# Optimization experiments

Hardware: AMD Instinct MI355X
Metric: run time of the kernel (lower is better)

## Reference

```python
import jax, jax.numpy as jnp
import numpy as np

MEDNUM = 50000
FEATDIM = 128
NNZ = 3200000
N = 2 * MEDNUM  # adjacency is over cat([mEmbed, mEmbed])


def setup_inputs() -> dict:
    key = jax.random.key(0)
    k1, k2, k3, k4, k5 = jax.random.split(key, 5)
    vals = jax.random.uniform(k1, (NNZ,), dtype=jnp.float32)
    mEmbed = jax.random.normal(k2, (MEDNUM, FEATDIM), dtype=jnp.float32)
    inter = jax.random.normal(k3, (1,), dtype=jnp.float32)
    row_idx = jax.random.randint(k4, (NNZ,), 0, N, dtype=jnp.int32)
    col_idx = jax.random.randint(k5, (NNZ,), 0, N, dtype=jnp.int32)
    return {"vals": vals, "mEmbed": mEmbed, "inter": inter,
            "row_idx": row_idx, "col_idx": col_idx}


def _gcn_layer(vals, row_idx, col_idx, embeds):
    # spmm(adj, embeds) via gather + weighted segment-sum, then LeakyReLU(0.5)
    gathered = embeds[col_idx] * vals[:, None]          # [E, F]
    agg = jax.ops.segment_sum(gathered, row_idx, num_segments=N)  # [N, F]
    return jnp.where(agg >= 0, agg, 0.5 * agg)          # LeakyReLU(negative_slope=0.5)


def reference(vals, mEmbed, inter, row_idx, col_idx):
    embeds1 = jnp.concatenate([mEmbed, mEmbed], axis=0)  # [2*mednum, F]
    # Source quirk: lats1 is never extended, so both iterations use embeds1.
    tem1 = jax.nn.relu(_gcn_layer(vals, row_idx, col_idx, embeds1))
    gnnEmbeds1 = tem1 + tem1                              # sum of two identical layers
    m1 = gnnEmbeds1[:MEDNUM]
    m2 = gnnEmbeds1[MEDNUM:]
    return inter * m1 + (1.0 - inter) * m2
```

## Files before the change

kernel.cpp:

```cpp
#include <hip/hip_runtime.h>

#define MEDNUM 50000
#define FEATDIM 128
#define NNZ 3200000
#define NBUCK 1563
#define SLAB 2304
#define PART_BLOCKS 250
#define PART_E 12800
#define PART_T 1024
#define PART_K 12
#define PART_TAIL 512
#define CAP SLAB

#define OFF_CUR    0
#define OFF_SCALE  1600
#define OFF_QT     51600
#define OFF_RECS   3251600


__global__ __launch_bounds__(256) void toint8_kernel(const float* __restrict__ mEmbed,
                                                     unsigned short* __restrict__ qt,
                                                     float* __restrict__ scales,
                                                     int* __restrict__ gcur) {
    int g = blockIdx.x * 256 + threadIdx.x;
    if (g < NBUCK) gcur[g] = g * SLAB;

    int row = blockIdx.x * 4 + (threadIdx.x >> 6);
    int lane = threadIdx.x & 63;
    if (row >= MEDNUM) return;
    float2 f = ((const float2*)(mEmbed + (long long)row * FEATDIM))[lane];
    float m = fmaxf(fabsf(f.x), fabsf(f.y));
    for (int o = 32; o > 0; o >>= 1) m = fmaxf(m, __shfl_xor(m, o, 64));
    float inv = (m > 0.f) ? 127.f / m : 0.f;
    float s   = (m > 0.f) ? m / 127.f : 0.f;
    int q0 = __float2int_rn(f.x * inv) + 128;
    int q1 = __float2int_rn(f.y * inv) + 128;
    qt[(long long)row * 64 + ((lane & 15) * 4 + (lane >> 4))] =
        (unsigned short)((q0 & 0xff) | ((q1 & 0xff) << 8));
    if (lane == 0) scales[row] = s;
}

__global__ __launch_bounds__(PART_T, 4) void part_kernel(const float* __restrict__ vals,
                                                         const int* __restrict__ row_idx,
                                                         const int* __restrict__ col_idx,
                                                         const float* __restrict__ scales,
                                                         int* __restrict__ gcur,
                                                         unsigned long long* __restrict__ recs) {
    __shared__ unsigned long long lrec[PART_E];
    __shared__ int lcnt[NBUCK];
    __shared__ int gstart[NBUCK];
    __shared__ int wsum[16];

    int tid = threadIdx.x;
    int base = blockIdx.x * PART_E;

    for (int i = tid; i < NBUCK; i += PART_T) lcnt[i] = 0;
    __syncthreads();

    unsigned long long rec[PART_K];
    unsigned long long rtail = 0;
    int have_tail = (tid < PART_TAIL);
    {
        int rr[PART_K], cc[PART_K];
        float vv[PART_K];
#pragma unroll
        for (int k = 0; k < PART_K; k++) {
            int e = base + k * PART_T + tid;
            rr[k] = __builtin_nontemporal_load(row_idx + e);
            cc[k] = __builtin_nontemporal_load(col_idx + e);
            vv[k] = __builtin_nontemporal_load(vals + e);
        }
        int rt = 0, ct = 0; float vt = 0.f;
        if (have_tail) {
            int e = base + PART_K * PART_T + tid;
            rt = __builtin_nontemporal_load(row_idx + e);
            ct = __builtin_nontemporal_load(col_idx + e);
            vt = __builtin_nontemporal_load(vals + e);
        }
        float ss[PART_K];
#pragma unroll
        for (int k = 0; k < PART_K; k++) {
            cc[k] = (cc[k] >= MEDNUM) ? cc[k] - MEDNUM : cc[k];
            ss[k] = scales[cc[k]];
        }
        float st = 0.f;
        if (have_tail) {
            ct = (ct >= MEDNUM) ? ct - MEDNUM : ct;
            st = scales[ct];
        }
#pragma unroll
        for (int k = 0; k < PART_K; k++) {
            int r = rr[k], half = 0;
            if (r >= MEDNUM) { r -= MEDNUM; half = 1; }
            float vp = vv[k] * ss[k];
            int b = r >> 5;
            int rib = (r & 31) | (half << 5);
            rec[k] = ((unsigned long long)__float_as_uint(vp) << 32)
                   | ((unsigned long long)(b >> 10) << 63)
                   | ((unsigned int)(b & 0x3FF) << 22)
                   | ((unsigned int)rib << 16)
                   | (unsigned int)cc[k];
            atomicAdd(&lcnt[b], 1);
        }
        if (have_tail) {
            int r = rt, half = 0;
            if (r >= MEDNUM) { r -= MEDNUM; half = 1; }
            float vp = vt * st;
            int b = r >> 5;
            int rib = (r & 31) | (half << 5);
            rtail = ((unsigned long long)__float_as_uint(vp) << 32)
                  | ((unsigned long long)(b >> 10) << 63)
                  | ((unsigned int)(b & 0x3FF) << 22)
                  | ((unsigned int)rib << 16)
                  | (unsigned int)ct;
            atomicAdd(&lcnt[b], 1);
        }
    }
    __syncthreads();

    int i0 = tid * 2;
    int c0 = 0, c1 = 0;
    if (i0 < NBUCK)     c0 = lcnt[i0];
    if (i0 + 1 < NBUCK) c1 = lcnt[i0 + 1];
    int s = c0 + c1;
    int x = s;
#pragma unroll
    for (int d = 1; d < 64; d <<= 1) {
        int t = __shfl_up(x, d, 64);
        if ((tid & 63) >= d) x += t;
    }
    int wave = tid >> 6, lane = tid & 63;
    if (lane == 63) wsum[wave] = x;
    __syncthreads();
    if (tid == 0) {
        int acc = 0;
#pragma unroll
        for (int w = 0; w < 16; w++) { int t = wsum[w]; wsum[w] = acc; acc += t; }
    }
    __syncthreads();
    int excl = wsum[wave] + x - s;

    {
        int e = excl;
        if (i0 < NBUCK) {
            if (c0 > 0) gstart[i0] = atomicAdd(&gcur[i0], c0) - e;
            lcnt[i0] = e;
            e += c0;
        }
        if (i0 + 1 < NBUCK) {
            if (c1 > 0) gstart[i0 + 1] = atomicAdd(&gcur[i0 + 1], c1) - e;
            lcnt[i0 + 1] = e;
            e += c1;
        }
    }
    __syncthreads();

#pragma unroll
    for (int k = 0; k < PART_K; k++) {
        unsigned long long r = rec[k];
        int b = (int)(((r >> 53) & 0x400u) | ((r >> 22) & 0x3FFu));
        int pos = atomicAdd(&lcnt[b], 1);
        lrec[pos] = r;
    }
    if (have_tail) {
        unsigned long long r = rtail;
        int b = (int)(((r >> 53) & 0x400u) | ((r >> 22) & 0x3FFu));
        int pos = atomicAdd(&lcnt[b], 1);
        lrec[pos] = r;
    }
    __syncthreads();

#pragma unroll
    for (int k = 0; k < PART_K; k++) {
        int j = k * PART_T + tid;
        unsigned long long r = lrec[j];
        int b = (int)(((r >> 53) & 0x400u) | ((r >> 22) & 0x3FFu));
        recs[gstart[b] + j] = r & 0x7FFFFFFFFFFFFFFFULL;
    }
    if (have_tail) {
        int j = PART_K * PART_T + tid;
        unsigned long long r = lrec[j];
        int b = (int)(((r >> 53) & 0x400u) | ((r >> 22) & 0x3FFu));
        recs[gstart[b] + j] = r & 0x7FFFFFFFFFFFFFFFULL;
    }
}

__device__ __forceinline__ void accum8_body(const unsigned int p[8],
                                            const unsigned short* __restrict__ qt,
                                            unsigned int flo,
                                            float acc[8], float& sv) {
    unsigned long long w[8];
#pragma unroll
    for (int q = 0; q < 8; q++)
        w[q] = *(const unsigned long long*)((const char*)qt
                   + (((p[q] & 0xffffu) << 7) | flo));
#pragma unroll
    for (int q = 0; q < 8; q++) {
        float v = __uint_as_float(p[q] & 0xffff0000u);
        sv += v;
        unsigned int wlo = (unsigned int)w[q], whi = (unsigned int)(w[q] >> 32);
        acc[0] = fmaf(v, (float)(wlo & 0xffu),         acc[0]);
        acc[1] = fmaf(v, (float)((wlo >> 8) & 0xffu),  acc[1]);
        acc[2] = fmaf(v, (float)((wlo >> 16) & 0xffu), acc[2]);
        acc[3] = fmaf(v, (float)(wlo >> 24),           acc[3]);
        acc[4] = fmaf(v, (float)(whi & 0xffu),         acc[4]);
        acc[5] = fmaf(v, (float)((whi >> 8) & 0xffu),  acc[5]);
        acc[6] = fmaf(v, (float)((whi >> 16) & 0xffu), acc[6]);
        acc[7] = fmaf(v, (float)(whi >> 24),           acc[7]);
    }
}

__device__ __forceinline__ void seg_to_pair(int s, int e,
                                            const unsigned int* __restrict__ st4,
                                            const unsigned short* __restrict__ qt,
                                            int qw, unsigned int flo,
                                            float& rx, float& ry) {
    float acc[8], sv;
#pragma unroll
    for (int x = 0; x < 8; x++) acc[x] = 0.f;
    sv = 0.f;
    int i = s;
    for (; i + 32 <= e; i += 32) {
        unsigned int p[8];
#pragma unroll
        for (int q = 0; q < 8; q++) p[q] = st4[i + q * 4 + qw];
        accum8_body(p, qt, flo, acc, sv);
    }
    if (i < e) {
        unsigned int p[8];
#pragma unroll
        for (int q = 0; q < 8; q++) {
            int j = i + q * 4 + qw;
            p[q] = (j < e) ? st4[j] : 0u;
        }
        accum8_body(p, qt, flo, acc, sv);
    }
#pragma unroll
    for (int x = 0; x < 8; x++) {
        acc[x] += __shfl_xor(acc[x], 16, 64);
        acc[x] += __shfl_xor(acc[x], 32, 64);
    }
    sv += __shfl_xor(sv, 16, 64);
    sv += __shfl_xor(sv, 32, 64);
    float sx = (qw & 2) ? ((qw & 1) ? acc[6] : acc[4]) : ((qw & 1) ? acc[2] : acc[0]);
    float sy = (qw & 2) ? ((qw & 1) ? acc[7] : acc[5]) : ((qw & 1) ? acc[3] : acc[1]);
    rx = fmaxf(fmaf(-128.f, sv, sx), 0.f);
    ry = fmaxf(fmaf(-128.f, sv, sy), 0.f);
}

__global__ __launch_bounds__(512, 6) void agg_kernel(const int* __restrict__ gcur,
                                                     const unsigned long long* __restrict__ recs,
                                                     const unsigned short* __restrict__ qt,
                                                     const float* __restrict__ inter,
                                                     float* __restrict__ out) {
    __shared__ unsigned long long slab8[CAP];
    __shared__ unsigned int st4[CAP];
    __shared__ int cnt[64];
    __shared__ int bas[65];
    int b = blockIdx.x, tid = threadIdx.x;
    long long gs = (long long)b * SLAB;
    int n = gcur[b] - b * SLAB;
    if (n > CAP) n = CAP;

    if (tid < 64) cnt[tid] = 0;
    __syncthreads();
    for (int j = tid; j < n; j += 512) {
        unsigned long long r = __builtin_nontemporal_load(recs + gs + j);
        slab8[j] = r;
        atomicAdd(&cnt[(int)((r >> 16) & 63)], 1);
    }
    __syncthreads();
    if (tid < 64) {
        int v = cnt[tid];
        int x = v;
#pragma unroll
        for (int d = 1; d < 64; d <<= 1) {
            int tmp = __shfl_up(x, d, 64);
            if (tid >= d) x += tmp;
        }
        bas[tid] = x - v;
        if (tid == 63) bas[64] = x;
        cnt[tid] = x - v;
    }
    __syncthreads();
    for (int j = tid; j < n; j += 512) {
        unsigned long long r = slab8[j];
        int rib = (int)((r >> 16) & 63);
        int p = atomicAdd(&cnt[rib], 1);
        unsigned int vb = (unsigned int)(r >> 32);
        vb = (vb + 0x7fffu + ((vb >> 16) & 1u)) & 0xffff0000u;
        st4[p] = ((unsigned int)(r & 0xffff)) | vb;
    }
    __syncthreads();
    float t = inter[0];
    float s1 = 2.f * t, s2 = 2.f * (1.f - t);
    int wave = tid >> 6, lane = tid & 63;
    int qw = lane >> 4;
    unsigned int flo = (unsigned int)((lane & 15) << 3);
#pragma unroll 1
    for (int i2 = 0; i2 < 4; i2++) {
        int rib0 = wave * 4 + i2;
        int frow = b * 32 + rib0;
        if (frow >= MEDNUM) break;
        float ax, ay, cx, cy;
        seg_to_pair(bas[rib0],      bas[rib0 + 1],  st4, qt, qw, flo, ax, ay);
        seg_to_pair(bas[rib0 + 32], bas[rib0 + 33], st4, qt, qw, flo, cx, cy);
        float ox = s1 * ax + s2 * cx;
        float oy = s1 * ay + s2 * cy;
        unsigned long long packed =
            (unsigned long long)__float_as_uint(ox)
          | ((unsigned long long)__float_as_uint(oy) << 32);
        __builtin_nontemporal_store(packed,
            (unsigned long long*)(out + (long long)frow * FEATDIM + lane * 2));
    }
}

extern "C" void kernel_launch(void* const* d_in, const int* in_sizes, int n_in,
                              void* d_out, int out_size, void* d_ws, size_t ws_size,
                              hipStream_t stream) {
    const float* vals    = (const float*)d_in[0];
    const float* mEmbed  = (const float*)d_in[1];
    const float* inter   = (const float*)d_in[2];
    const int*   row_idx = (const int*)d_in[3];
    const int*   col_idx = (const int*)d_in[4];
    float* out = (float*)d_out;

    int* ws = (int*)d_ws;
    int* gcur = ws + OFF_CUR;
    float* scales = (float*)(ws + OFF_SCALE);
    unsigned short* qt = (unsigned short*)(ws + OFF_QT);
    unsigned long long* recs = (unsigned long long*)(ws + OFF_RECS);

    toint8_kernel<<<(MEDNUM + 3) / 4, 256, 0, stream>>>(mEmbed, qt, scales, gcur);
    part_kernel<<<PART_BLOCKS, PART_T, 0, stream>>>(vals, row_idx, col_idx, scales, gcur, recs);
    agg_kernel<<<NBUCK, 512, 0, stream>>>(gcur, recs, qt, inter, out);
}
```

Before: 198.2 us.

## Replace int8 per-row-scaled embedding table with fp16 and fma_mix accumulation

Stores the embedding table as fp16 instead of int8 with per-row scales, and accumulates with v_fma_mix_f32 straight from packed halves. This removes the scale gather in the partition kernel, the byte-extract and convert work, and the offset-correction sum in the aggregation. In exchange each gathered row is twice as many bytes (16-byte loads per lane), and the inner unroll drops from 8 to 6 edges per step. Accuracy should also improve over the int8 quantisation.

```diff
diff --git a/kernel.cpp b/kernel.cpp
--- a/kernel.cpp
+++ b/kernel.cpp
@@ -1,4 +1,5 @@
 #include <hip/hip_runtime.h>
+#include <hip/hip_fp16.h>
 
 #define MEDNUM 50000
 #define FEATDIM 128
@@ -18,9 +19,17 @@
 #define OFF_RECS   3251600
 
 
-__global__ __launch_bounds__(256) void toint8_kernel(const float* __restrict__ mEmbed,
-                                                     unsigned short* __restrict__ qt,
-                                                     float* __restrict__ scales,
+__device__ __forceinline__ void fmamix_lo(float& acc, float v, unsigned int w) {
+    asm("v_fma_mix_f32 %0, %1, %2, %0 op_sel:[0,0,0] op_sel_hi:[0,1,0]"
+        : "+v"(acc) : "v"(v), "v"(w));
+}
+__device__ __forceinline__ void fmamix_hi(float& acc, float v, unsigned int w) {
+    asm("v_fma_mix_f32 %0, %1, %2, %0 op_sel:[0,1,0] op_sel_hi:[0,1,0]"
+        : "+v"(acc) : "v"(v), "v"(w));
+}
+
+__global__ __launch_bounds__(256) void tofp16_kernel(const float* __restrict__ mEmbed,
+                                                     unsigned int* __restrict__ qt,
                                                      int* __restrict__ gcur) {
     int g = blockIdx.x * 256 + threadIdx.x;
     if (g < NBUCK) gcur[g] = g * SLAB;
@@ -29,21 +38,14 @@
     int lane = threadIdx.x & 63;
     if (row >= MEDNUM) return;
     float2 f = ((const float2*)(mEmbed + (long long)row * FEATDIM))[lane];
-    float m = fmaxf(fabsf(f.x), fabsf(f.y));
-    for (int o = 32; o > 0; o >>= 1) m = fmaxf(m, __shfl_xor(m, o, 64));
-    float inv = (m > 0.f) ? 127.f / m : 0.f;
-    float s   = (m > 0.f) ? m / 127.f : 0.f;
-    int q0 = __float2int_rn(f.x * inv) + 128;
-    int q1 = __float2int_rn(f.y * inv) + 128;
-    qt[(long long)row * 64 + ((lane & 15) * 4 + (lane >> 4))] =
-        (unsigned short)((q0 & 0xff) | ((q1 & 0xff) << 8));
-    if (lane == 0) scales[row] = s;
+    unsigned int h0 = __half_as_ushort(__float2half(f.x));
+    unsigned int h1 = __half_as_ushort(__float2half(f.y));
+    qt[(long long)row * 64 + 4 * (lane & 15) + (lane >> 4)] = h0 | (h1 << 16);
 }
 
 __global__ __launch_bounds__(PART_T, 4) void part_kernel(const float* __restrict__ vals,
                                                          const int* __restrict__ row_idx,
                                                          const int* __restrict__ col_idx,
-                                                         const float* __restrict__ scales,
                                                          int* __restrict__ gcur,
                                                          unsigned long long* __restrict__ recs) {
     __shared__ unsigned long long lrec[PART_E];
@@ -77,25 +79,14 @@
             ct = __builtin_nontemporal_load(col_idx + e);
             vt = __builtin_nontemporal_load(vals + e);
         }
-        float ss[PART_K];
 #pragma unroll
         for (int k = 0; k < PART_K; k++) {
             cc[k] = (cc[k] >= MEDNUM) ? cc[k] - MEDNUM : cc[k];
-            ss[k] = scales[cc[k]];
-        }
-        float st = 0.f;
-        if (have_tail) {
-            ct = (ct >= MEDNUM) ? ct - MEDNUM : ct;
-            st = scales[ct];
-        }
-#pragma unroll
-        for (int k = 0; k < PART_K; k++) {
             int r = rr[k], half = 0;
             if (r >= MEDNUM) { r -= MEDNUM; half = 1; }
-            float vp = vv[k] * ss[k];
             int b = r >> 5;
             int rib = (r & 31) | (half << 5);
-            rec[k] = ((unsigned long long)__float_as_uint(vp) << 32)
+            rec[k] = ((unsigned long long)__float_as_uint(vv[k]) << 32)
                    | ((unsigned long long)(b >> 10) << 63)
                    | ((unsigned int)(b & 0x3FF) << 22)
                    | ((unsigned int)rib << 16)
@@ -103,12 +94,12 @@
             atomicAdd(&lcnt[b], 1);
         }
         if (have_tail) {
+            ct = (ct >= MEDNUM) ? ct - MEDNUM : ct;
             int r = rt, half = 0;
             if (r >= MEDNUM) { r -= MEDNUM; half = 1; }
-            float vp = vt * st;
             int b = r >> 5;
             int rib = (r & 31) | (half << 5);
-            rtail = ((unsigned long long)__float_as_uint(vp) << 32)
+            rtail = ((unsigned long long)__float_as_uint(vt) << 32)
                   | ((unsigned long long)(b >> 10) << 63)
                   | ((unsigned int)(b & 0x3FF) << 22)
                   | ((unsigned int)rib << 16)
@@ -185,72 +176,62 @@
     }
 }
 
-__device__ __forceinline__ void accum8_body(const unsigned int p[8],
-                                            const unsigned short* __restrict__ qt,
+__device__ __forceinline__ void accum6_body(const unsigned int p[6],
+                                            const unsigned int* __restrict__ qt,
                                             unsigned int flo,
-                                            float acc[8], float& sv) {
-    unsigned long long w[8];
-#pragma unroll
-    for (int q = 0; q < 8; q++)
-        w[q] = *(const unsigned long long*)((const char*)qt
-                   + (((p[q] & 0xffffu) << 7) | flo));
-#pragma unroll
-    for (int q = 0; q < 8; q++) {
+                                            float acc[8]) {
+    uint4 W[6];
+#pragma unroll
+    for (int q = 0; q < 6; q++)
+        W[q] = *(const uint4*)((const char*)qt + (((p[q] & 0xffffu) << 8) | flo));
+#pragma unroll
+    for (int q = 0; q < 6; q++) {
         float v = __uint_as_float(p[q] & 0xffff0000u);
-        sv += v;
-        unsigned int wlo = (unsigned int)w[q], whi = (unsigned int)(w[q] >> 32);
-        acc[0] = fmaf(v, (float)(wlo & 0xffu),         acc[0]);
-        acc[1] = fmaf(v, (float)((wlo >> 8) & 0xffu),  acc[1]);
-        acc[2] = fmaf(v, (float)((wlo >> 16) & 0xffu), acc[2]);
-        acc[3] = fmaf(v, (float)(wlo >> 24),           acc[3]);
-        acc[4] = fmaf(v, (float)(whi & 0xffu),         acc[4]);
-        acc[5] = fmaf(v, (float)((whi >> 8) & 0xffu),  acc[5]);
-        acc[6] = fmaf(v, (float)((whi >> 16) & 0xffu), acc[6]);
-        acc[7] = fmaf(v, (float)(whi >> 24),           acc[7]);
+        fmamix_lo(acc[0], v, W[q].x); fmamix_hi(acc[1], v, W[q].x);
+        fmamix_lo(acc[2], v, W[q].y); fmamix_hi(acc[3], v, W[q].y);
+        fmamix_lo(acc[4], v, W[q].z); fmamix_hi(acc[5], v, W[q].z);
+        fmamix_lo(acc[6], v, W[q].w); fmamix_hi(acc[7], v, W[q].w);
     }
 }
 
 __device__ __forceinline__ void seg_to_pair(int s, int e,
                                             const unsigned int* __restrict__ st4,
-                                            const unsigned short* __restrict__ qt,
+                                            const unsigned int* __restrict__ qt,
                                             int qw, unsigned int flo,
                                             float& rx, float& ry) {
-    float acc[8], sv;
+    float acc[8];
 #pragma unroll
     for (int x = 0; x < 8; x++) acc[x] = 0.f;
-    sv = 0.f;
     int i = s;
-    for (; i + 32 <= e; i += 32) {
-        unsigned int p[8];
-#pragma unroll
-        for (int q = 0; q < 8; q++) p[q] = st4[i + q * 4 + qw];
-        accum8_body(p, qt, flo, acc, sv);
+    for (; i + 24 <= e; i += 24) {
+        unsigned int p[6];
+#pragma unroll
+        for (int q = 0; q < 6; q++) p[q] = st4[i + q * 4 + qw];
+        accum6_body(p, qt, flo, acc);
     }
     if (i < e) {
-        unsigned int p[8];
-#pragma unroll
-        for (int q = 0; q < 8; q++) {
+        unsigned int p[6];
+#pragma unroll
+        for (int q = 0; q < 6; q++) {
             int j = i + q * 4 + qw;
             p[q] = (j < e) ? st4[j] : 0u;
         }
-        accum8_body(p, qt, flo, acc, sv);
+        accum6_body(p, qt, flo, acc);
     }
 #pragma unroll
     for (int x = 0; x < 8; x++) {
         acc[x] += __shfl_xor(acc[x], 16, 64);
         acc[x] += __shfl_xor(acc[x], 32, 64);
     }
-    sv += __shfl_xor(sv, 16, 64);
-    sv += __shfl_xor(sv, 32, 64);
     float sx = (qw & 2) ? ((qw & 1) ? acc[6] : acc[4]) : ((qw & 1) ? acc[2] : acc[0]);
     float sy = (qw & 2) ? ((qw & 1) ? acc[7] : acc[5]) : ((qw & 1) ? acc[3] : acc[1]);
-    rx = fmaxf(fmaf(-128.f, sv, sx), 0.f);
-    ry = fmaxf(fmaf(-128.f, sv, sy), 0.f);
+    rx = fmaxf(sx, 0.f);
+    ry = fmaxf(sy, 0.f);
 }
 
 __global__ __launch_bounds__(512, 6) void agg_kernel(const int* __restrict__ gcur,
                                                      const unsigned long long* __restrict__ recs,
-                                                     const unsigned short* __restrict__ qt,
+                                                     const unsigned int* __restrict__ qt,
                                                      const float* __restrict__ inter,
                                                      float* __restrict__ out) {
     __shared__ unsigned long long slab8[CAP];
@@ -296,7 +277,7 @@
     float s1 = 2.f * t, s2 = 2.f * (1.f - t);
     int wave = tid >> 6, lane = tid & 63;
     int qw = lane >> 4;
-    unsigned int flo = (unsigned int)((lane & 15) << 3);
+    unsigned int flo = (unsigned int)((lane & 15) << 4);
 #pragma unroll 1
     for (int i2 = 0; i2 < 4; i2++) {
         int rib0 = wave * 4 + i2;
@@ -327,11 +308,10 @@
 
     int* ws = (int*)d_ws;
     int* gcur = ws + OFF_CUR;
-    float* scales = (float*)(ws + OFF_SCALE);
-    unsigned short* qt = (unsigned short*)(ws + OFF_QT);
+    unsigned int* qt = (unsigned int*)(ws + OFF_QT);
     unsigned long long* recs = (unsigned long long*)(ws + OFF_RECS);
 
-    toint8_kernel<<<(MEDNUM + 3) / 4, 256, 0, stream>>>(mEmbed, qt, scales, gcur);
-    part_kernel<<<PART_BLOCKS, PART_T, 0, stream>>>(vals, row_idx, col_idx, scales, gcur, recs);
+    tofp16_kernel<<<(MEDNUM + 3) / 4, 256, 0, stream>>>(mEmbed, qt, gcur);
+    part_kernel<<<PART_BLOCKS, PART_T, 0, stream>>>(vals, row_idx, col_idx, gcur, recs);
     agg_kernel<<<NBUCK, 512, 0, stream>>>(gcur, recs, qt, inter, out);
 }
```

Result: slower. 244.4 us (+23.3%).

## Split quantized embedding table into two column halves processed in separate passes

Applied to the files above, without the earlier changes.

The int8 embedding table is split into two halves by column index (rows below and above 25000), and the record column field now carries a half bit. The aggregation kernel bins edges by destination row and column half, then runs two passes over the halves, summing partial results before the ReLU and output scaling. Each pass gathers from a half-size table, which is meant to improve cache locality for the random gathers. In exchange it adds twice as many segment loops, a smaller inner unroll (4 instead of 8 gathers in flight), and extra scan and binning work.

```diff
diff --git a/kernel.cpp b/kernel.cpp
--- a/kernel.cpp
+++ b/kernel.cpp
@@ -1,6 +1,7 @@
 #include <hip/hip_runtime.h>
 
 #define MEDNUM 50000
+#define COLH 25000
 #define FEATDIM 128
 #define NNZ 3200000
 #define NBUCK 1563
@@ -35,7 +36,9 @@
     float s   = (m > 0.f) ? m / 127.f : 0.f;
     int q0 = __float2int_rn(f.x * inv) + 128;
     int q1 = __float2int_rn(f.y * inv) + 128;
-    qt[(long long)row * 64 + ((lane & 15) * 4 + (lane >> 4))] =
+    int h = (row >= COLH);
+    int rm = row - (h ? COLH : 0);
+    qt[h * 1600000 + rm * 64 + ((lane & 15) * 4 + (lane >> 4))] =
         (unsigned short)((q0 & 0xff) | ((q1 & 0xff) << 8));
     if (lane == 0) scales[row] = s;
 }
@@ -95,11 +98,14 @@
             float vp = vv[k] * ss[k];
             int b = r >> 5;
             int rib = (r & 31) | (half << 5);
+            int c = cc[k];
+            int ch = (c >= COLH);
+            unsigned int colfield = (unsigned int)(c - (ch ? COLH : 0)) | ((unsigned int)ch << 15);
             rec[k] = ((unsigned long long)__float_as_uint(vp) << 32)
                    | ((unsigned long long)(b >> 10) << 63)
                    | ((unsigned int)(b & 0x3FF) << 22)
                    | ((unsigned int)rib << 16)
-                   | (unsigned int)cc[k];
+                   | colfield;
             atomicAdd(&lcnt[b], 1);
         }
         if (have_tail) {
@@ -108,11 +114,13 @@
             float vp = vt * st;
             int b = r >> 5;
             int rib = (r & 31) | (half << 5);
+            int ch = (ct >= COLH);
+            unsigned int colfield = (unsigned int)(ct - (ch ? COLH : 0)) | ((unsigned int)ch << 15);
             rtail = ((unsigned long long)__float_as_uint(vp) << 32)
                   | ((unsigned long long)(b >> 10) << 63)
                   | ((unsigned int)(b & 0x3FF) << 22)
                   | ((unsigned int)rib << 16)
-                  | (unsigned int)ct;
+                  | colfield;
             atomicAdd(&lcnt[b], 1);
         }
     }
@@ -185,17 +193,16 @@
     }
 }
 
-__device__ __forceinline__ void accum8_body(const unsigned int p[8],
-                                            const unsigned short* __restrict__ qt,
+__device__ __forceinline__ void accum4_body(const unsigned int p[4],
+                                            const unsigned char* __restrict__ qb,
                                             unsigned int flo,
                                             float acc[8], float& sv) {
-    unsigned long long w[8];
-#pragma unroll
-    for (int q = 0; q < 8; q++)
-        w[q] = *(const unsigned long long*)((const char*)qt
-                   + (((p[q] & 0xffffu) << 7) | flo));
-#pragma unroll
-    for (int q = 0; q < 8; q++) {
+    unsigned long long w[4];
+#pragma unroll
+    for (int q = 0; q < 4; q++)
+        w[q] = *(const unsigned long long*)(qb + (((p[q] & 0x7fffu) << 7) | flo));
+#pragma unroll
+    for (int q = 0; q < 4; q++) {
         float v = __uint_as_float(p[q] & 0xffff0000u);
         sv += v;
         unsigned int wlo = (unsigned int)w[q], whi = (unsigned int)(w[q] >> 32);
@@ -210,30 +217,29 @@
     }
 }
 
-__device__ __forceinline__ void seg_to_pair(int s, int e,
-                                            const unsigned int* __restrict__ st4,
-                                            const unsigned short* __restrict__ qt,
-                                            int qw, unsigned int flo,
-                                            float& rx, float& ry) {
-    float acc[8], sv;
+__device__ __forceinline__ void seg_pair(int s, int e,
+                                         const unsigned int* __restrict__ st4,
+                                         const unsigned char* __restrict__ qb,
+                                         int qw, unsigned int flo,
+                                         float& rx, float& ry) {
+    float acc[8], sv = 0.f;
 #pragma unroll
     for (int x = 0; x < 8; x++) acc[x] = 0.f;
-    sv = 0.f;
     int i = s;
-    for (; i + 32 <= e; i += 32) {
-        unsigned int p[8];
-#pragma unroll
-        for (int q = 0; q < 8; q++) p[q] = st4[i + q * 4 + qw];
-        accum8_body(p, qt, flo, acc, sv);
+    for (; i + 16 <= e; i += 16) {
+        unsigned int p[4];
+#pragma unroll
+        for (int q = 0; q < 4; q++) p[q] = st4[i + q * 4 + qw];
+        accum4_body(p, qb, flo, acc, sv);
     }
     if (i < e) {
-        unsigned int p[8];
-#pragma unroll
-        for (int q = 0; q < 8; q++) {
+        unsigned int p[4];
+#pragma unroll
+        for (int q = 0; q < 4; q++) {
             int j = i + q * 4 + qw;
             p[q] = (j < e) ? st4[j] : 0u;
         }
-        accum8_body(p, qt, flo, acc, sv);
+        accum4_body(p, qb, flo, acc, sv);
     }
 #pragma unroll
     for (int x = 0; x < 8; x++) {
@@ -244,8 +250,8 @@
     sv += __shfl_xor(sv, 32, 64);
     float sx = (qw & 2) ? ((qw & 1) ? acc[6] : acc[4]) : ((qw & 1) ? acc[2] : acc[0]);
     float sy = (qw & 2) ? ((qw & 1) ? acc[7] : acc[5]) : ((qw & 1) ? acc[3] : acc[1]);
-    rx = fmaxf(fmaf(-128.f, sv, sx), 0.f);
-    ry = fmaxf(fmaf(-128.f, sv, sy), 0.f);
+    rx = fmaf(-128.f, sv, sx);
+    ry = fmaf(-128.f, sv, sy);
 }
 
 __global__ __launch_bounds__(512, 6) void agg_kernel(const int* __restrict__ gcur,
@@ -255,38 +261,43 @@
                                                      float* __restrict__ out) {
     __shared__ unsigned long long slab8[CAP];
     __shared__ unsigned int st4[CAP];
-    __shared__ int cnt[64];
-    __shared__ int bas[65];
+    __shared__ int cnt[128];
+    __shared__ int bas[129];
     int b = blockIdx.x, tid = threadIdx.x;
     long long gs = (long long)b * SLAB;
     int n = gcur[b] - b * SLAB;
     if (n > CAP) n = CAP;
 
-    if (tid < 64) cnt[tid] = 0;
+    if (tid < 128) cnt[tid] = 0;
     __syncthreads();
     for (int j = tid; j < n; j += 512) {
         unsigned long long r = __builtin_nontemporal_load(recs + gs + j);
         slab8[j] = r;
-        atomicAdd(&cnt[(int)((r >> 16) & 63)], 1);
+        int bin = (int)((r >> 16) & 63) | (((int)(r >> 15) & 1) << 6);
+        atomicAdd(&cnt[bin], 1);
     }
     __syncthreads();
     if (tid < 64) {
-        int v = cnt[tid];
-        int x = v;
+        int c0 = cnt[2 * tid], c1 = cnt[2 * tid + 1];
+        int s = c0 + c1;
+        int x = s;
 #pragma unroll
         for (int d = 1; d < 64; d <<= 1) {
             int tmp = __shfl_up(x, d, 64);
             if (tid >= d) x += tmp;
         }
-        bas[tid] = x - v;
-        if (tid == 63) bas[64] = x;
-        cnt[tid] = x - v;
+        int excl = x - s;
+        bas[2 * tid] = excl;
+        bas[2 * tid + 1] = excl + c0;
+        if (tid == 63) bas[128] = x;
+        cnt[2 * tid] = excl;
+        cnt[2 * tid + 1] = excl + c0;
     }
     __syncthreads();
     for (int j = tid; j < n; j += 512) {
         unsigned long long r = slab8[j];
-        int rib = (int)((r >> 16) & 63);
-        int p = atomicAdd(&cnt[rib], 1);
+        int bin = (int)((r >> 16) & 63) | (((int)(r >> 15) & 1) << 6);
+        int p = atomicAdd(&cnt[bin], 1);
         unsigned int vb = (unsigned int)(r >> 32);
         vb = (vb + 0x7fffu + ((vb >> 16) & 1u)) & 0xffff0000u;
         st4[p] = ((unsigned int)(r & 0xffff)) | vb;
@@ -297,16 +308,29 @@
     int wave = tid >> 6, lane = tid & 63;
     int qw = lane >> 4;
     unsigned int flo = (unsigned int)((lane & 15) << 3);
-#pragma unroll 1
+    float pax[4], pay[4], pcx[4], pcy[4];
+#pragma unroll
+    for (int h = 0; h < 2; h++) {
+        const unsigned char* qb = (const unsigned char*)qt + h * 3200000;
+#pragma unroll
+        for (int i2 = 0; i2 < 4; i2++) {
+            int rib0 = wave * 4 + i2;
+            int frow = b * 32 + rib0;
+            if (frow >= MEDNUM) continue;
+            float ax, ay, cx, cy;
+            seg_pair(bas[h * 64 + rib0],      bas[h * 64 + rib0 + 1],  st4, qb, qw, flo, ax, ay);
+            seg_pair(bas[h * 64 + rib0 + 32], bas[h * 64 + rib0 + 33], st4, qb, qw, flo, cx, cy);
+            if (h == 0) { pax[i2] = ax;  pay[i2] = ay;  pcx[i2] = cx;  pcy[i2] = cy; }
+            else        { pax[i2] += ax; pay[i2] += ay; pcx[i2] += cx; pcy[i2] += cy; }
+        }
+    }
+#pragma unroll
     for (int i2 = 0; i2 < 4; i2++) {
         int rib0 = wave * 4 + i2;
         int frow = b * 32 + rib0;
-        if (frow >= MEDNUM) break;
-        float ax, ay, cx, cy;
-        seg_to_pair(bas[rib0],      bas[rib0 + 1],  st4, qt, qw, flo, ax, ay);
-        seg_to_pair(bas[rib0 + 32], bas[rib0 + 33], st4, qt, qw, flo, cx, cy);
-        float ox = s1 * ax + s2 * cx;
-        float oy = s1 * ay + s2 * cy;
+        if (frow >= MEDNUM) continue;
+        float ox = s1 * fmaxf(pax[i2], 0.f) + s2 * fmaxf(pcx[i2], 0.f);
+        float oy = s1 * fmaxf(pay[i2], 0.f) + s2 * fmaxf(pcy[i2], 0.f);
         unsigned long long packed =
             (unsigned long long)__float_as_uint(ox)
           | ((unsigned long long)__float_as_uint(oy) << 32);
```

Result: slower. 293.9 us (+48.3%).
